# Kernel tuning notes

Measured on AMD Instinct MI355X. Metric: run time of the kernel, lower is better.

Reference implementation:

```python
import jax, jax.numpy as jnp
import numpy as np
import math

D = 1024
H = 16
HD = D // H

def layernorm(x, g, b, eps=1e-5):
    mu = jnp.mean(x, axis=-1, keepdims=True)
    var = jnp.var(x, axis=-1, keepdims=True)
    return (x - mu) * jax.lax.rsqrt(var + eps) * g + b

def setup_inputs() -> dict:
    key = jax.random.key(0)
    ks = jax.random.split(key, 12)
    s = 0.02
    return {
        "x": jax.random.normal(ks[0], (2, 2048, D), jnp.float32),
        "Wk": jax.random.normal(ks[1], (D, D), jnp.float32) * s,
        "Wq": jax.random.normal(ks[2], (D, D), jnp.float32) * s,
        "Wv": jax.random.normal(ks[3], (D, D), jnp.float32) * s,
        "Wp": jax.random.normal(ks[4], (D, D), jnp.float32) * s,
        "bp": jnp.zeros((D,), jnp.float32),
        "g1": jnp.ones((D,), jnp.float32),
        "b1": jnp.zeros((D,), jnp.float32),
        "g2": jnp.ones((D,), jnp.float32),
        "b2": jnp.zeros((D,), jnp.float32),
        "W1": jax.random.normal(ks[5], (D, 4 * D), jnp.float32) * s,
        "bm1": jnp.zeros((4 * D,), jnp.float32),
        "W2": jax.random.normal(ks[6], (4 * D, D), jnp.float32) * s,
        "bm2": jnp.zeros((D,), jnp.float32),
    }

def reference(x, Wk, Wq, Wv, Wp, bp, g1, b1, g2, b2, W1, bm1, W2, bm2):
    B, S, _ = x.shape
    xn = layernorm(x, g1, b1)  # pre-LN; residual uses xn (faithful to source)
    # project and split heads -> [B, H, S, HD]
    def heads(y):
        return y.reshape(B, S, H, HD).transpose(0, 2, 1, 3)
    q = heads(xn @ Wq)
    k = heads(xn @ Wk)
    v = heads(xn @ Wv)
    scale = 1.0 / math.sqrt(HD)
    att = jnp.einsum('bhsd,bhtd->bhst', q, k) * scale  # [B,H,S,S]
    diag = jnp.eye(S, dtype=bool)
    att = jnp.where(diag, -jnp.inf, att)  # exclude self-attention on diagonal
    att = jax.nn.softmax(att, axis=-1)
    y = jnp.einsum('bhst,bhtd->bhsd', att, v)
    y = y.transpose(0, 2, 1, 3).reshape(B, S, D)
    y = y @ Wp + bp  # dropout is identity at inference
    h = xn + y
    hn = layernorm(h, g2, b2)
    mlp = jax.nn.gelu(hn @ W1 + bm1, approximate=False) @ W2 + bm2
    return h + mlp
```

## Files before the change

kernel.cpp:

```cpp
#include <hip/hip_runtime.h>
#include <hip/hip_bf16.h>
#include <math.h>

#define BATCH   2
#define SEQ     2048
#define D_MODEL 1024
#define NHEAD   16
#define HEADD   64
#define NROWS   (BATCH * SEQ)
#define D_FF    4096
#define TPARTS  4
#define TSPAN   (SEQ / TPARTS)

typedef __bf16 bf16_t;
typedef __bf16 bf16x2 __attribute__((ext_vector_type(2)));
typedef __bf16 bf16x4 __attribute__((ext_vector_type(4)));
typedef __bf16 bf16x8 __attribute__((ext_vector_type(8)));
typedef float  f32x4  __attribute__((ext_vector_type(4)));

#define QSCALE 0.18033688011112042f

__device__ __forceinline__ void gload_lds16(const void* g, void* l) {
    __builtin_amdgcn_global_load_lds(
        (const __attribute__((address_space(1))) unsigned int*)g,
        (__attribute__((address_space(3))) unsigned int*)l, 16, 0, 0);
}

__global__ __launch_bounds__(256) void transpose_all6(
    const float* __restrict__ Wq, const float* __restrict__ Wk,
    const float* __restrict__ Wv, const float* __restrict__ Wp,
    const float* __restrict__ W1, const float* __restrict__ W2,
    bf16_t* __restrict__ Wqkvt, bf16_t* __restrict__ Wpt,
    bf16_t* __restrict__ W1t, bf16_t* __restrict__ W2t)
{
    __shared__ float tile[32][33];
    int bid = blockIdx.x;
    const float* W; bf16_t* Wt; int K, N, n0, k0;
    if (bid < 4096) {
        int seg = bid >> 10, t = bid & 1023;
        W  = (seg == 0) ? Wq : (seg == 1) ? Wk : (seg == 2) ? Wv : Wp;
        Wt = (seg < 3) ? (Wqkvt + (size_t)seg * 1024 * 1024) : Wpt;
        K = 1024; N = 1024;
        n0 = (t & 31) * 32; k0 = (t >> 5) * 32;
    } else if (bid < 8192) {
        int t = bid - 4096;
        W = W1; Wt = W1t; K = 1024; N = 4096;
        n0 = (t & 127) * 32; k0 = (t >> 7) * 32;
    } else {
        int t = bid - 8192;
        W = W2; Wt = W2t; K = 4096; N = 1024;
        n0 = (t & 31) * 32; k0 = (t >> 5) * 32;
    }
    int tx = threadIdx.x;
    int ty = threadIdx.y;
    #pragma unroll
    for (int i = 0; i < 32; i += 8)
        tile[ty + i][tx] = W[(size_t)(k0 + ty + i) * N + n0 + tx];
    __syncthreads();
    #pragma unroll
    for (int i = 0; i < 32; i += 8)
        Wt[(size_t)(n0 + ty + i) * K + k0 + tx] = (bf16_t)tile[tx][ty + i];
}

__global__ __launch_bounds__(256) void ln_kernel(
    const float* __restrict__ x, const float* __restrict__ g,
    const float* __restrict__ b, bf16_t* __restrict__ out)
{
    int row = blockIdx.x;
    int tid = threadIdx.x;
    const float* xr = x + (size_t)row * D_MODEL;
    f32x4 v = *(const f32x4*)(xr + tid * 4);
    float s  = v[0] + v[1] + v[2] + v[3];
    float s2 = v[0]*v[0] + v[1]*v[1] + v[2]*v[2] + v[3]*v[3];
    #pragma unroll
    for (int off = 32; off; off >>= 1) {
        s  += __shfl_down(s, off);
        s2 += __shfl_down(s2, off);
    }
    __shared__ float ps[4], ps2[4];
    int w = tid >> 6, lane = tid & 63;
    if (lane == 0) { ps[w] = s; ps2[w] = s2; }
    __syncthreads();
    float sum  = ps[0] + ps[1] + ps[2] + ps[3];
    float sum2 = ps2[0] + ps2[1] + ps2[2] + ps2[3];
    float mu  = sum * (1.0f / D_MODEL);
    float var = sum2 * (1.0f / D_MODEL) - mu * mu;
    float rs  = rsqrtf(var + 1e-5f);
    #pragma unroll
    for (int j = 0; j < 4; ++j) {
        int c = tid * 4 + j;
        out[(size_t)row * D_MODEL + c] = (bf16_t)((v[j] - mu) * rs * g[c] + b[c]);
    }
}

template<int EPI, int BN>
__global__ __launch_bounds__(256) void gemm128(
    const bf16_t* __restrict__ A, const bf16_t* __restrict__ Bt,
    const float* __restrict__ bias, const void* __restrict__ resid,
    void* __restrict__ out, int M, int N, int K, int RY)
{
    constexpr int JN = BN / 32;
    constexpr int NBUF = (BN == 64) ? 3 : 2;
    __shared__ bf16_t As[NBUF][128 * 64];
    __shared__ bf16_t Bs[NBUF][BN * 64];
    int tid = threadIdx.x;
    int bid = blockIdx.x;
    int cx = bid & 3, cy = (bid >> 2) & 1, i0 = bid >> 3;
    int m0 = ((cx << 3) + (i0 & 7)) << 7;
    int n0 = (cy * RY + (i0 >> 3)) * BN;
    int w = tid >> 6, lane = tid & 63, quad = lane >> 4, l15 = lane & 15;
    int wm = (w & 1) * 64, wn = (w >> 1) * (BN / 2);
    int srow = tid >> 3;
    int sxor = (((tid & 7) ^ (srow & 7)) << 3);

    const bf16_t* Ap = A  + (size_t)(m0 + srow) * K + sxor;
    const bf16_t* Bp = Bt + (size_t)(n0 + srow) * K + sxor;

    int rxs = l15 & 7;

    auto stage = [&](int buf, int k0) {
        bf16_t* AsW = &As[buf][w * 512];
        bf16_t* BsW = &Bs[buf][w * 512];
        #pragma unroll
        for (int p = 0; p < 4; ++p)
            gload_lds16(Ap + (size_t)p * 32 * K + k0, AsW + p * 2048);
        #pragma unroll
        for (int p = 0; p < JN; ++p)
            gload_lds16(Bp + (size_t)p * 32 * K + k0, BsW + p * 2048);
    };

    f32x4 acc[4][JN] = {};

    int nt = K >> 6;
    stage(0, 0);
    if (NBUF == 3 && nt > 1) stage(1, 64);
    for (int t = 0; t < nt; ++t) {
        int cur = t % NBUF;
        if constexpr (NBUF == 3) {
            if (t + 2 < nt) {
                stage((t + 2) % NBUF, (t + 2) << 6);
                asm volatile("s_waitcnt vmcnt(12)" ::: "memory");
            } else if (t + 1 < nt) {
                asm volatile("s_waitcnt vmcnt(6)" ::: "memory");
            } else {
                asm volatile("s_waitcnt vmcnt(0)" ::: "memory");
            }
        } else {
            if (t + 1 < nt) {
                stage((t + 1) % NBUF, (t + 1) << 6);
                asm volatile("s_waitcnt vmcnt(8)" ::: "memory");
            } else {
                asm volatile("s_waitcnt vmcnt(0)" ::: "memory");
            }
        }
        __builtin_amdgcn_s_barrier();
        __builtin_amdgcn_sched_barrier(0);
        #pragma unroll
        for (int kk = 0; kk < 2; ++kk) {
            bf16x8 af[4], bfr[JN];
            #pragma unroll
            for (int i = 0; i < 4; ++i)
                af[i] = *(const bf16x8*)&As[cur][(wm + i * 16 + l15) * 64
                                            + ((((kk << 2) | quad) ^ rxs) << 3)];
            #pragma unroll
            for (int j = 0; j < JN; ++j)
                bfr[j] = *(const bf16x8*)&Bs[cur][(wn + j * 16 + l15) * 64
                                            + ((((kk << 2) | quad) ^ rxs) << 3)];
            #pragma unroll
            for (int i = 0; i < 4; ++i)
                #pragma unroll
                for (int j = 0; j < JN; ++j)
                    acc[i][j] = __builtin_amdgcn_mfma_f32_16x16x32_bf16(af[i], bfr[j], acc[i][j], 0, 0, 0);
        }
        __builtin_amdgcn_sched_barrier(0);
        asm volatile("s_waitcnt lgkmcnt(0)" ::: "memory");
        __builtin_amdgcn_s_barrier();
        __builtin_amdgcn_sched_barrier(0);
    }

    #pragma unroll
    for (int i = 0; i < 4; ++i)
    #pragma unroll
    for (int j = 0; j < JN; ++j) {
        int col  = n0 + wn + j * 16 + l15;
        int row0 = m0 + wm + i * 16 + quad * 4;
        if (EPI == 6) {
            int region = (n0 + wn + j * 16) >> 10;
            if (region < 2) {
                #pragma unroll
                for (int r = 0; r < 4; ++r) {
                    int row = row0 + r;
                    float v = acc[i][j][r];
                    if (region == 0) v *= QSCALE;
                    int b = row >> 11, s = row & 2047, hh = (col & 1023) >> 6, d = col & 63;
                    bf16_t* dst = (bf16_t*)out + (size_t)region * 4194304;
                    dst[(((size_t)(b * NHEAD + hh)) * SEQ + s) * HEADD + d] = (bf16_t)v;
                }
            } else {
                int dg = col - 2048, hh = dg >> 6, d = dg & 63;
                int b = row0 >> 11, s0 = row0 & 2047;
                bf16x4 pv;
                #pragma unroll
                for (int r = 0; r < 4; ++r) pv[r] = (bf16_t)acc[i][j][r];
                *(bf16x4*)((bf16_t*)out + 8388608
                           + (((size_t)(b * NHEAD + hh)) * HEADD + d) * SEQ + s0) = pv;
            }
        } else {
            float bv = bias[col];
            #pragma unroll
            for (int r = 0; r < 4; ++r) {
                int row = row0 + r;
                float vacc = acc[i][j][r] + bv;
                if (EPI == 1) {
                    float res = (float)((const bf16_t*)resid)[(size_t)row * N + col];
                    ((float*)out)[(size_t)row * N + col] = vacc + res;
                } else if (EPI == 2) {
                    float u = vacc;
                    float y = u * (0.7978845608028654f + 0.03567740814f * u * u);
                    float e = __builtin_amdgcn_exp2f(2.8853900817779268f * y);
                    float r8 = __builtin_amdgcn_rcpf(e + 1.0f);
                    ((bf16_t*)out)[(size_t)row * N + col] = (bf16_t)(u - u * r8);
                } else {
                    float res = ((const float*)resid)[(size_t)row * N + col];
                    ((float*)out)[(size_t)row * N + col] = vacc + res;
                }
            }
        }
    }
}

__global__ __launch_bounds__(256, 4) void attn_kernel(
    const bf16_t* __restrict__ q, const bf16_t* __restrict__ k,
    const bf16_t* __restrict__ vt, bf16_t* __restrict__ po,
    float* __restrict__ plsum)
{
    int gid = blockIdx.x;
    int xcd = gid & 7;
    int loc = gid >> 3;
    int bh  = xcd * 4 + (loc >> 6);
    int rest = loc & 63;
    int qt   = rest >> 2;
    int part = rest & 3;
    int tb0 = part * TSPAN, tend = tb0 + TSPAN;
    int b = bh >> 4, h = bh & 15;
    int tid = threadIdx.x, w = tid >> 6, lane = tid & 63;
    int quad = lane >> 4, l15 = lane & 15;
    int qbase = qt * 128 + w * 32;
    const bf16_t* qh = q  + (size_t)bh * SEQ * HEADD;
    const bf16_t* kh = k  + (size_t)bh * SEQ * HEADD;
    const bf16_t* vh = vt + (size_t)bh * HEADD * SEQ;

    bf16x8 qa[2][2];
    #pragma unroll
    for (int m = 0; m < 2; ++m)
        #pragma unroll
        for (int hf = 0; hf < 2; ++hf)
            qa[m][hf] = *(const bf16x8*)(qh + (size_t)(qbase + m * 16 + l15) * HEADD + hf * 32 + quad * 8);

    bf16x8 ones;
    #pragma unroll
    for (int j = 0; j < 8; ++j) ones[j] = (bf16_t)1.0f;

    __shared__ alignas(16) bf16_t Ks[32 * 72];
    __shared__ alignas(16) bf16_t Vs[64 * 40];
    __shared__ alignas(16) bf16_t Pl[4][32][40];

    int ksrow = tid >> 3, kscol = (tid & 7) * 8;
    int vsrow = tid >> 2, vscol = (tid & 3) * 8;
    const bf16_t* kg = kh + (size_t)ksrow * HEADD + kscol;
    const bf16_t* vg = vh + (size_t)vsrow * SEQ + vscol;

    f32x4 o[2][4] = {};
    f32x4 ls[2] = {};

    for (int t0 = tb0; t0 < tend; t0 += 32) {
        bf16x8 kreg = *(const bf16x8*)(kg + (size_t)t0 * HEADD);
        bf16x8 vreg = *(const bf16x8*)(vg + t0);
        __syncthreads();
        *(bf16x8*)&Ks[ksrow * 72 + kscol] = kreg;
        *(bf16x8*)&Vs[vsrow * 40 + vscol] = vreg;
        __syncthreads();

        bf16x8 kb[2][2], vf[4];
        #pragma unroll
        for (int jt = 0; jt < 2; ++jt)
            #pragma unroll
            for (int hf = 0; hf < 2; ++hf)
                kb[jt][hf] = *(const bf16x8*)&Ks[(2 * l15 + jt) * 72 + hf * 32 + quad * 8];
        #pragma unroll
        for (int dn = 0; dn < 4; ++dn)
            vf[dn] = *(const bf16x8*)&Vs[(dn * 16 + l15) * 40 + quad * 8];

        #pragma unroll
        for (int m = 0; m < 2; ++m) {
            f32x4 sc[2];
            #pragma unroll
            for (int jt = 0; jt < 2; ++jt) {
                f32x4 z = {};
                z = __builtin_amdgcn_mfma_f32_16x16x32_bf16(qa[m][0], kb[jt][0], z, 0, 0, 0);
                z = __builtin_amdgcn_mfma_f32_16x16x32_bf16(qa[m][1], kb[jt][1], z, 0, 0, 0);
                sc[jt] = z;
            }
            int qm = qbase + m * 16;
            bool dg = (t0 < qm + 16) && (t0 + 32 > qm);
            #pragma unroll
            for (int r = 0; r < 4; ++r) {
                int qrow = qm + quad * 4 + r;
                float p0 = __builtin_amdgcn_exp2f(sc[0][r]);
                float p1 = __builtin_amdgcn_exp2f(sc[1][r]);
                if (dg) {
                    int tg = t0 + 2 * l15;
                    if (tg == qrow)     p0 = 0.0f;
                    if (tg + 1 == qrow) p1 = 0.0f;
                }
                bf16x2 pp = { (bf16_t)p0, (bf16_t)p1 };
                *(bf16x2*)&Pl[w][m * 16 + quad * 4 + r][2 * l15] = pp;
            }
        }
        #pragma unroll
        for (int m = 0; m < 2; ++m) {
            bf16x8 pf = *(const bf16x8*)&Pl[w][m * 16 + l15][quad * 8];
            ls[m] = __builtin_amdgcn_mfma_f32_16x16x32_bf16(pf, ones, ls[m], 0, 0, 0);
            #pragma unroll
            for (int dn = 0; dn < 4; ++dn)
                o[m][dn] = __builtin_amdgcn_mfma_f32_16x16x32_bf16(pf, vf[dn], o[m][dn], 0, 0, 0);
        }
    }

    #pragma unroll
    for (int m = 0; m < 2; ++m)
        #pragma unroll
        for (int dn = 0; dn < 4; ++dn)
            #pragma unroll
            for (int r = 0; r < 4; ++r) {
                int qrow = qbase + m * 16 + quad * 4 + r;
                po[(((size_t)part * NROWS) + b * SEQ + qrow) * D_MODEL
                   + h * HEADD + dn * 16 + l15] = (bf16_t)o[m][dn][r];
            }
    if (l15 == 0) {
        #pragma unroll
        for (int m = 0; m < 2; ++m)
            #pragma unroll
            for (int r = 0; r < 4; ++r) {
                int qrow = qbase + m * 16 + quad * 4 + r;
                plsum[((size_t)part * 32 + bh) * SEQ + qrow] = ls[m][r];
            }
    }
}

__global__ __launch_bounds__(256) void attn_merge(
    const bf16_t* __restrict__ po, const float* __restrict__ plsum,
    bf16_t* __restrict__ y)
{
    int row = blockIdx.x;
    int tid = threadIdx.x;
    int c = tid * 4;
    int b = row >> 11, s = row & 2047;
    int bh = b * NHEAD + (c >> 6);
    float l = 0.0f;
    f32x4 ov = {};
    #pragma unroll
    for (int p = 0; p < TPARTS; ++p) {
        l += plsum[((size_t)p * 32 + bh) * SEQ + s];
        bf16x4 t = *(const bf16x4*)&po[((size_t)p * NROWS + row) * D_MODEL + c];
        #pragma unroll
        for (int j = 0; j < 4; ++j) ov[j] += (float)t[j];
    }
    float rl = 1.0f / l;
    bf16x4 out;
    #pragma unroll
    for (int j = 0; j < 4; ++j) out[j] = (bf16_t)(ov[j] * rl);
    *(bf16x4*)&y[(size_t)row * D_MODEL + c] = out;
}

extern "C" void kernel_launch(void* const* d_in, const int* in_sizes, int n_in,
                              void* d_out, int out_size, void* d_ws, size_t ws_size,
                              hipStream_t stream)
{
    const float* x   = (const float*)d_in[0];
    const float* Wk  = (const float*)d_in[1];
    const float* Wq  = (const float*)d_in[2];
    const float* Wv  = (const float*)d_in[3];
    const float* Wp  = (const float*)d_in[4];
    const float* bp  = (const float*)d_in[5];
    const float* g1  = (const float*)d_in[6];
    const float* b1  = (const float*)d_in[7];
    const float* g2  = (const float*)d_in[8];
    const float* b2  = (const float*)d_in[9];
    const float* W1  = (const float*)d_in[10];
    const float* bm1 = (const float*)d_in[11];
    const float* W2  = (const float*)d_in[12];
    const float* bm2 = (const float*)d_in[13];

    char* ws = (char*)d_ws;
    const size_t MB = 1024 * 1024;
    bf16_t* Wqkvt = (bf16_t*)(ws + 0 * MB);
    bf16_t* Wpt = (bf16_t*)(ws + 6 * MB);
    bf16_t* W1t = (bf16_t*)(ws + 8 * MB);
    bf16_t* W2t = (bf16_t*)(ws + 16 * MB);
    bf16_t* xn  = (bf16_t*)(ws + 24 * MB);
    bf16_t* qkv = (bf16_t*)(ws + 32 * MB);
    bf16_t* qb  = (bf16_t*)(ws + 32 * MB);
    bf16_t* kb  = (bf16_t*)(ws + 40 * MB);
    bf16_t* vtb = (bf16_t*)(ws + 48 * MB);
    bf16_t* yb  = (bf16_t*)(ws + 56 * MB);
    float*  hbuf= (float*) (ws + 64 * MB);
    bf16_t* po  = (bf16_t*)(ws + 64 * MB);
    float*  pls = (float*) (ws + 96 * MB);
    bf16_t* hn  = (bf16_t*)(ws + 24 * MB);
    bf16_t* act = (bf16_t*)(ws + 32 * MB);

    transpose_all6<<<12288, dim3(32, 8), 0, stream>>>(
        Wq, Wk, Wv, Wp, W1, W2, Wqkvt, Wpt, W1t, W2t);

    ln_kernel<<<NROWS, 256, 0, stream>>>(x, g1, b1, xn);

    gemm128<6, 128><<<768, 256, 0, stream>>>(xn, Wqkvt, nullptr, nullptr, qkv, NROWS, 3072, D_MODEL, 12);

    attn_kernel<<<2048, 256, 0, stream>>>(qb, kb, vtb, po, pls);
    attn_merge<<<NROWS, 256, 0, stream>>>(po, pls, yb);

    gemm128<1, 64><<<512, 256, 0, stream>>>(yb, Wpt, bp, xn, hbuf, NROWS, D_MODEL, D_MODEL, 8);

    ln_kernel<<<NROWS, 256, 0, stream>>>(hbuf, g2, b2, hn);

    gemm128<2, 128><<<1024, 256, 0, stream>>>(hn, W1t, bm1, nullptr, act, NROWS, D_FF, D_MODEL, 16);
    gemm128<3, 64><<<512, 256, 0, stream>>>(act, W2t, bm2, hbuf, d_out, NROWS, D_MODEL, D_FF, 8);
}
```

Baseline: 347.7 us.

## Use dedicated 256x256-tile GEMM kernel with 8 waves for MLP up-projection with GELU

Replaces the 128x128-tile gemm128 for the W1 projection (4096x4096x1024) with a new 512-thread kernel computing 256x256 tiles, where each wave owns a 128x64 subtile. Operands are double-buffered in LDS via direct global-to-LDS loads, prefetches are split across MMA phases, and s_setprio is raised around the MFMA blocks. The larger tile raises arithmetic intensity and data reuse per LDS load. In exchange the grid shrinks to 256 blocks, about one per CU, and the kernel uses 128KB of LDS plus large register accumulators, which limits occupancy and latency hiding.

```diff
diff --git a/kernel.cpp b/kernel.cpp
--- a/kernel.cpp
+++ b/kernel.cpp
@@ -93,6 +93,125 @@
     }
 }
 
+__global__ __launch_bounds__(512) void gemm256_gelu(
+    const bf16_t* __restrict__ A, const bf16_t* __restrict__ Bt,
+    const float* __restrict__ bias, bf16_t* __restrict__ out,
+    int M, int N, int K)
+{
+    __shared__ bf16_t As[2][256 * 64];
+    __shared__ bf16_t Bs[2][256 * 64];
+    int tid = threadIdx.x;
+    int bid = blockIdx.x;
+    int m0 = (bid & 15) * 256;
+    int n0 = (bid >> 4) * 256;
+    int w = tid >> 6, lane = tid & 63, quad = lane >> 4, l15 = lane & 15;
+    int wm = (w >> 2) * 128;
+    int wn = (w & 3) * 64;
+    int rxs = l15 & 7;
+
+    int srow = tid >> 3;
+    int sxor = (((tid & 7) ^ (srow & 7)) << 3);
+    const bf16_t* Ap = A  + (size_t)(m0 + srow) * K + sxor;
+    const bf16_t* Bp = Bt + (size_t)(n0 + srow) * K + sxor;
+
+    f32x4 acc[8][4] = {};
+
+    int nt = K >> 6;
+    {
+        bf16_t* AsW = &As[0][w * 512];
+        bf16_t* BsW = &Bs[0][w * 512];
+        #pragma unroll
+        for (int h = 0; h < 2; ++h)
+            #pragma unroll
+            for (int p = 0; p < 2; ++p) {
+                gload_lds16(Ap + (size_t)(h * 128 + p * 64) * K, AsW + h * 8192 + p * 4096);
+                gload_lds16(Bp + (size_t)(h * 128 + p * 64) * K, BsW + h * 8192 + p * 4096);
+            }
+    }
+
+    for (int t = 0; t < nt; ++t) {
+        int cur = t & 1;
+        const bf16_t* Asc = &As[cur][0];
+        const bf16_t* Bsc = &Bs[cur][0];
+        bf16_t* AsN = &As[cur ^ 1][w * 512];
+        bf16_t* BsN = &Bs[cur ^ 1][w * 512];
+        bool pf = (t + 1 < nt);
+        int k1 = (t + 1) << 6;
+        asm volatile("s_waitcnt vmcnt(0)" ::: "memory");
+        __builtin_amdgcn_s_barrier();
+        __builtin_amdgcn_sched_barrier(0);
+
+        bf16x8 bfr[4][2];
+        #pragma unroll
+        for (int q = 0; q < 4; ++q) {
+            bf16x8 af[2][2];
+            #pragma unroll
+            for (int ii = 0; ii < 2; ++ii)
+                #pragma unroll
+                for (int kk = 0; kk < 2; ++kk)
+                    af[ii][kk] = *(const bf16x8*)&Asc[(wm + (2 * q + ii) * 16 + l15) * 64
+                                                      + (((kk * 4 + quad) ^ rxs) << 3)];
+            if (q == 0) {
+                #pragma unroll
+                for (int j = 0; j < 4; ++j)
+                    #pragma unroll
+                    for (int kk = 0; kk < 2; ++kk)
+                        bfr[j][kk] = *(const bf16x8*)&Bsc[(wn + j * 16 + l15) * 64
+                                                          + (((kk * 4 + quad) ^ rxs) << 3)];
+            }
+            if (q == 0 && pf) {
+                #pragma unroll
+                for (int h = 0; h < 2; ++h)
+                    #pragma unroll
+                    for (int p = 0; p < 2; ++p)
+                        gload_lds16(Ap + (size_t)(h * 128 + p * 64) * K + k1,
+                                    AsN + h * 8192 + p * 4096);
+            }
+            if (q == 1 && pf) {
+                #pragma unroll
+                for (int h = 0; h < 2; ++h)
+                    #pragma unroll
+                    for (int p = 0; p < 2; ++p)
+                        gload_lds16(Bp + (size_t)(h * 128 + p * 64) * K + k1,
+                                    BsN + h * 8192 + p * 4096);
+            }
+            __builtin_amdgcn_s_barrier();
+            asm volatile("s_waitcnt lgkmcnt(0)" ::: "memory");
+            __builtin_amdgcn_sched_barrier(0);
+            __builtin_amdgcn_s_setprio(1);
+            #pragma unroll
+            for (int ii = 0; ii < 2; ++ii)
+                #pragma unroll
+                for (int j = 0; j < 4; ++j)
+                    #pragma unroll
+                    for (int kk = 0; kk < 2; ++kk)
+                        acc[2 * q + ii][j] = __builtin_amdgcn_mfma_f32_16x16x32_bf16(
+                            af[ii][kk], bfr[j][kk], acc[2 * q + ii][j], 0, 0, 0);
+            __builtin_amdgcn_s_setprio(0);
+            __builtin_amdgcn_sched_barrier(0);
+            __builtin_amdgcn_s_barrier();
+        }
+    }
+
+    #pragma unroll
+    for (int i = 0; i < 8; ++i)
+    #pragma unroll
+    for (int j = 0; j < 4; ++j) {
+        int col  = n0 + wn + j * 16 + l15;
+        int row0 = m0 + wm + i * 16 + quad * 4;
+        float bv = bias[col];
+        #pragma unroll
+        for (int r = 0; r < 4; ++r) {
+            int row = row0 + r;
+            float u = acc[i][j][r] + bv;
+            float y = u * (0.7978845608028654f + 0.03567740814f * u * u);
+            float e = __builtin_amdgcn_exp2f(2.8853900817779268f * y);
+            float r8 = __builtin_amdgcn_rcpf(e + 1.0f);
+            out[(size_t)row * N + col] = (bf16_t)(u - u * r8);
+        }
+    }
+}
+
 template<int EPI, int BN>
 __global__ __launch_bounds__(256) void gemm128(
     const bf16_t* __restrict__ A, const bf16_t* __restrict__ Bt,
@@ -214,12 +333,6 @@
                 if (EPI == 1) {
                     float res = (float)((const bf16_t*)resid)[(size_t)row * N + col];
                     ((float*)out)[(size_t)row * N + col] = vacc + res;
-                } else if (EPI == 2) {
-                    float u = vacc;
-                    float y = u * (0.7978845608028654f + 0.03567740814f * u * u);
-                    float e = __builtin_amdgcn_exp2f(2.8853900817779268f * y);
-                    float r8 = __builtin_amdgcn_rcpf(e + 1.0f);
-                    ((bf16_t*)out)[(size_t)row * N + col] = (bf16_t)(u - u * r8);
                 } else {
                     float res = ((const float*)resid)[(size_t)row * N + col];
                     ((float*)out)[(size_t)row * N + col] = vacc + res;
@@ -424,6 +537,6 @@
 
     ln_kernel<<<NROWS, 256, 0, stream>>>(hbuf, g2, b2, hn);
 
-    gemm128<2, 128><<<1024, 256, 0, stream>>>(hn, W1t, bm1, nullptr, act, NROWS, D_FF, D_MODEL, 16);
+    gemm256_gelu<<<256, 512, 0, stream>>>(hn, W1t, bm1, act, NROWS, D_FF, D_MODEL);
     gemm128<3, 64><<<512, 256, 0, stream>>>(act, W2t, bm2, hbuf, d_out, NROWS, D_MODEL, D_FF, 8);
 }
```

Result: no change. 343.6 us (-1.2%).
